# Kernel tuning notes

Hardware: AMD Instinct MI355X
Metric: run time of the kernel (lower is better)

The kernel has to match this reference:

```python
import jax, jax.numpy as jnp
import numpy as np


def setup_inputs() -> dict:
    key = jax.random.key(0)
    ks = jax.random.split(key, 3)
    B, H, W, C = 32, 56, 56, 512
    N = H * W
    x = jax.random.normal(ks[0], (B, N, C), dtype=jnp.float32)
    # learned params (qkv_bias=False)
    w_qkv = jax.random.normal(ks[1], (C, 3 * C), dtype=jnp.float32) * (C ** -0.5)
    w_proj = jax.random.normal(ks[2], (C, C), dtype=jnp.float32) * (C ** -0.5)
    b_proj = jnp.zeros((C,), dtype=jnp.float32)
    return {"x": x, "w_qkv": w_qkv, "w_proj": w_proj, "b_proj": b_proj,
            "H": H, "W": W}


def reference(x, w_qkv, w_proj, b_proj, H, W):
    num_heads, ws = 8, 7
    B, N, C = x.shape
    hd = C // num_heads
    scale = hd ** -0.5
    hg, wg = H // ws, W // ws
    G = hg * wg  # total groups
    S = ws * ws  # tokens per window
    # window partition: [B,N,C] -> [B,G,S,C]
    xw = x.reshape(B, hg, ws, wg, ws, C).transpose(0, 1, 3, 2, 4, 5)
    xw = xw.reshape(B, G, S, C)
    # qkv projection -> [3,B,G,heads,S,hd]
    qkv = (xw @ w_qkv).reshape(B, G, S, 3, num_heads, hd)
    qkv = qkv.transpose(3, 0, 1, 4, 2, 5)
    q, k, v = qkv[0], qkv[1], qkv[2]
    attn = jnp.einsum('bghqd,bghkd->bghqk', q, k) * scale
    attn = jax.nn.softmax(attn, axis=-1)
    out = jnp.einsum('bghqk,bghkd->bghqd', attn, v)
    # merge heads: [B,G,h,S,d] -> [B,G,S,C]
    out = out.transpose(0, 1, 3, 2, 4).reshape(B, G, S, C)
    # window merge: [B,G,S,C] -> [B,N,C]
    out = out.reshape(B, hg, wg, ws, ws, C).transpose(0, 1, 3, 2, 4, 5)
    out = out.reshape(B, N, C)
    return out @ w_proj + b_proj
```

## Files before the change

### kernel.cpp

```cpp
#include <hip/hip_runtime.h>

typedef unsigned short ushort;
typedef unsigned int uint;
typedef __bf16 bf16x8 __attribute__((ext_vector_type(8)));
typedef unsigned short u16x8 __attribute__((ext_vector_type(8)));
typedef float f32x4 __attribute__((ext_vector_type(4)));

__device__ __forceinline__ ushort f2bf(float f) {
  uint u = __builtin_bit_cast(uint, f);
  u += 0x7fffu + ((u >> 16) & 1u);
  return (ushort)(u >> 16);
}

__device__ __forceinline__ f32x4 mfma_bf16(u16x8 a, u16x8 b, f32x4 c) {
  return __builtin_amdgcn_mfma_f32_16x16x32_bf16(
      __builtin_bit_cast(bf16x8, a), __builtin_bit_cast(bf16x8, b), c, 0, 0, 0);
}

__global__ __launch_bounds__(256) void cvt_x(const float* __restrict__ X,
                                             ushort* __restrict__ Xb, int total8) {
  int stride = gridDim.x * 256;
  for (int i = blockIdx.x * 256 + threadIdx.x; i < total8; i += stride) {
    f32x4 a = ((const f32x4*)X)[2 * i];
    f32x4 b = ((const f32x4*)X)[2 * i + 1];
    u16x8 o;
#pragma unroll
    for (int j = 0; j < 4; ++j) { o[j] = f2bf(a[j]); o[j + 4] = f2bf(b[j]); }
    ((u16x8*)Xb)[i] = o;
  }
}

__global__ __launch_bounds__(256) void transpose_cvt(const float* __restrict__ W,
                                                     ushort* __restrict__ WT,
                                                     int K, int N) {
  __shared__ float t[32][33];
  const int tn0 = blockIdx.x * 32, tk0 = blockIdx.y * 32;
  const int tx = threadIdx.x & 31, ty = threadIdx.x >> 5;
#pragma unroll
  for (int i = 0; i < 4; ++i) {
    int k = tk0 + ty + i * 8;
    t[ty + i * 8][tx] = W[(size_t)k * N + tn0 + tx];
  }
  __syncthreads();
#pragma unroll
  for (int i = 0; i < 4; ++i) {
    int n = tn0 + ty + i * 8;
    WT[(size_t)n * K + tk0 + tx] = f2bf(t[tx][ty + i * 8]);
  }
}

__global__ __launch_bounds__(256) void gemm_qkv2(const ushort* __restrict__ A,
                                                 const ushort* __restrict__ BT,
                                                 ushort* __restrict__ C) {
  __shared__ __align__(16) ushort as_[128 * 32];
  __shared__ __align__(16) ushort bs_[128 * 32];
  const int tid = threadIdx.x;
  const int lane = tid & 63;
  const int wid = tid >> 6;
  const int c16 = lane & 15, q4 = lane >> 4;
  const int m0 = blockIdx.x * 128, n0 = blockIdx.y * 128;
  const int wr = (wid >> 1) * 64, wc = (wid & 1) * 64;

  f32x4 acc[4][4];
#pragma unroll
  for (int m = 0; m < 4; ++m)
#pragma unroll
    for (int n = 0; n < 4; ++n) acc[m][n] = f32x4{0.f, 0.f, 0.f, 0.f};

  const ushort* aptr = A + (size_t)(m0 + (tid >> 2)) * 512 + (tid & 3) * 8;
  const ushort* bptr = BT + (size_t)(n0 + (tid >> 2)) * 512 + (tid & 3) * 8;
  auto al0 = (__attribute__((address_space(3))) uint*)(as_ + tid * 8);
  auto al1 = (__attribute__((address_space(3))) uint*)(as_ + 2048 + tid * 8);
  auto bl0 = (__attribute__((address_space(3))) uint*)(bs_ + tid * 8);
  auto bl1 = (__attribute__((address_space(3))) uint*)(bs_ + 2048 + tid * 8);
  const ushort* ard = as_ + (wr + c16) * 32 + q4 * 8;
  const ushort* brd = bs_ + (wc + c16) * 32 + q4 * 8;

  for (int k0 = 0; k0 < 512; k0 += 32) {
    if (k0) __syncthreads();
    __builtin_amdgcn_global_load_lds(
        (__attribute__((address_space(1))) uint*)(aptr + k0), al0, 16, 0, 0);
    __builtin_amdgcn_global_load_lds(
        (__attribute__((address_space(1))) uint*)(aptr + 64 * 512 + k0), al1, 16, 0, 0);
    __builtin_amdgcn_global_load_lds(
        (__attribute__((address_space(1))) uint*)(bptr + k0), bl0, 16, 0, 0);
    __builtin_amdgcn_global_load_lds(
        (__attribute__((address_space(1))) uint*)(bptr + 64 * 512 + k0), bl1, 16, 0, 0);
    __syncthreads();
    u16x8 af[4], bf[4];
#pragma unroll
    for (int m = 0; m < 4; ++m) af[m] = *reinterpret_cast<const u16x8*>(ard + m * 512);
#pragma unroll
    for (int n = 0; n < 4; ++n) bf[n] = *reinterpret_cast<const u16x8*>(brd + n * 512);
#pragma unroll
    for (int m = 0; m < 4; ++m)
#pragma unroll
      for (int n = 0; n < 4; ++n) acc[m][n] = mfma_bf16(af[m], bf[n], acc[m][n]);
  }
  const int row0 = m0 + wr + q4 * 4;
  const int col0 = n0 + wc + c16;
#pragma unroll
  for (int m = 0; m < 4; ++m)
#pragma unroll
    for (int r = 0; r < 4; ++r) {
      ushort* cp = C + (size_t)(row0 + m * 16 + r) * 1536 + col0;
      cp[0]  = f2bf(acc[m][0][r]);
      cp[16] = f2bf(acc[m][1][r]);
      cp[32] = f2bf(acc[m][2][r]);
      cp[48] = f2bf(acc[m][3][r]);
    }
}

__global__ __launch_bounds__(256) void attn_win(const ushort* __restrict__ qkv,
                                                ushort* __restrict__ O) {
  __shared__ __align__(16) ushort p_lds[4][4096];
  __shared__ __align__(16) ushort v_lds[4][4096];
  const int tid = threadIdx.x, lane = tid & 63, w = tid >> 6;
  const int wg = blockIdx.x * 4 + w;
  const int head = wg & 7, g = (wg >> 3) & 63, b = wg >> 9;
  const int gh = g >> 3, gw = g & 7;
  const int c16 = lane & 15, q4 = lane >> 4;
  const size_t brow = (size_t)b * 3136;
  const u16x8 Z = {0, 0, 0, 0, 0, 0, 0, 0};

  int rowq[4]; bool val[4];
#pragma unroll
  for (int i = 0; i < 4; ++i) {
    int s = i * 16 + c16;
    val[i] = (s < 49);
    int ss = val[i] ? s : 0;
    rowq[i] = (gh * 7 + ss / 7) * 56 + gw * 7 + ss % 7;
  }
  const int qc = head * 64 + q4 * 8;

  u16x8 qf[2][4], kf[2][4];
#pragma unroll
  for (int i = 0; i < 4; ++i) {
    const ushort* p = qkv + (brow + rowq[i]) * 1536 + qc;
#pragma unroll
    for (int kk = 0; kk < 2; ++kk) {
      qf[kk][i] = val[i] ? *reinterpret_cast<const u16x8*>(p + kk * 32) : Z;
      kf[kk][i] = val[i] ? *reinterpret_cast<const u16x8*>(p + 512 + kk * 32) : Z;
    }
  }

  {
    int t = lane < 49 ? lane : 0;
    const ushort* vp =
        qkv + (brow + ((gh * 7 + t / 7) * 56 + gw * 7 + t % 7)) * 1536 + 1024 + head * 64;
    u16x8 vr[8];
#pragma unroll
    for (int j = 0; j < 8; ++j)
      vr[j] = (lane < 49) ? *reinterpret_cast<const u16x8*>(vp + j * 8) : Z;
#pragma unroll
    for (int d = 0; d < 64; ++d)
      v_lds[w][(d * 64 + lane) ^ ((d & 7) << 3)] = vr[d >> 3][d & 7];
  }

  f32x4 acc[4][4];
#pragma unroll
  for (int m = 0; m < 4; ++m)
#pragma unroll
    for (int n = 0; n < 4; ++n) acc[m][n] = f32x4{0.f, 0.f, 0.f, 0.f};
#pragma unroll
  for (int kk = 0; kk < 2; ++kk)
#pragma unroll
    for (int m = 0; m < 4; ++m)
#pragma unroll
      for (int n = 0; n < 4; ++n)
        acc[m][n] = mfma_bf16(qf[kk][m], kf[kk][n], acc[m][n]);

#pragma unroll
  for (int m = 0; m < 4; ++m)
#pragma unroll
    for (int r = 0; r < 4; ++r) {
      float s0 = acc[m][0][r] * 0.125f;
      float s1 = acc[m][1][r] * 0.125f;
      float s2 = acc[m][2][r] * 0.125f;
      float s3 = (c16 == 0) ? acc[m][3][r] * 0.125f : -1e30f;
      float mx = fmaxf(fmaxf(s0, s1), fmaxf(s2, s3));
#pragma unroll
      for (int off = 1; off < 16; off <<= 1) mx = fmaxf(mx, __shfl_xor(mx, off));
      s0 = __expf(s0 - mx);
      s1 = __expf(s1 - mx);
      s2 = __expf(s2 - mx);
      s3 = (c16 == 0) ? __expf(s3 - mx) : 0.f;
      float sum = s0 + s1 + s2 + s3;
#pragma unroll
      for (int off = 1; off < 16; off <<= 1) sum += __shfl_xor(sum, off);
      float inv = 1.f / sum;
      int row = m * 16 + q4 * 4 + r;
      int rb = row * 64, sw = (row & 7) << 3;
      p_lds[w][(rb + c16) ^ sw]      = f2bf(s0 * inv);
      p_lds[w][(rb + 16 + c16) ^ sw] = f2bf(s1 * inv);
      p_lds[w][(rb + 32 + c16) ^ sw] = f2bf(s2 * inv);
      p_lds[w][(rb + 48 + c16) ^ sw] = f2bf(s3 * inv);
    }
  __syncthreads();

  f32x4 o[4][4];
#pragma unroll
  for (int m = 0; m < 4; ++m)
#pragma unroll
    for (int n = 0; n < 4; ++n) o[m][n] = f32x4{0.f, 0.f, 0.f, 0.f};
#pragma unroll
  for (int kk = 0; kk < 2; ++kk) {
    u16x8 pa[4], vb[4];
#pragma unroll
    for (int m = 0; m < 4; ++m) {
      int row = m * 16 + c16;
      pa[m] = *reinterpret_cast<const u16x8*>(
          &p_lds[w][(row * 64 + kk * 32 + q4 * 8) ^ ((row & 7) << 3)]);
    }
#pragma unroll
    for (int n = 0; n < 4; ++n) {
      int d = n * 16 + c16;
      vb[n] = *reinterpret_cast<const u16x8*>(
          &v_lds[w][(d * 64 + kk * 32 + q4 * 8) ^ ((d & 7) << 3)]);
    }
#pragma unroll
    for (int m = 0; m < 4; ++m)
#pragma unroll
      for (int n = 0; n < 4; ++n) o[m][n] = mfma_bf16(pa[m], vb[n], o[m][n]);
  }

#pragma unroll
  for (int m = 0; m < 4; ++m)
#pragma unroll
    for (int r = 0; r < 4; ++r) {
      int s = m * 16 + q4 * 4 + r;
      if (s < 49) {
        int n_tok = (gh * 7 + s / 7) * 56 + gw * 7 + s % 7;
        ushort* op = O + (brow + n_tok) * 512 + head * 64 + c16;
        op[0]  = f2bf(o[m][0][r]);
        op[16] = f2bf(o[m][1][r]);
        op[32] = f2bf(o[m][2][r]);
        op[48] = f2bf(o[m][3][r]);
      }
    }
}

__global__ __launch_bounds__(256) void gemm_proj(const ushort* __restrict__ A,
                                                 const ushort* __restrict__ BT,
                                                 const float* __restrict__ bias,
                                                 float* __restrict__ C) {
  __shared__ __align__(16) ushort as_[128 * 32];
  __shared__ __align__(16) ushort bs_[128 * 32];
  const int tid = threadIdx.x;
  const int lane = tid & 63;
  const int wid = tid >> 6;
  const int c16 = lane & 15, q4 = lane >> 4;
  const int m0 = blockIdx.x * 128, n0 = blockIdx.y * 128;
  const int wr = (wid >> 1) * 64, wc = (wid & 1) * 64;

  f32x4 acc[4][4];
#pragma unroll
  for (int m = 0; m < 4; ++m)
#pragma unroll
    for (int n = 0; n < 4; ++n) acc[m][n] = f32x4{0.f, 0.f, 0.f, 0.f};

  const ushort* aptr = A + (size_t)(m0 + (tid >> 2)) * 512 + (tid & 3) * 8;
  const ushort* bptr = BT + (size_t)(n0 + (tid >> 2)) * 512 + (tid & 3) * 8;
  auto al0 = (__attribute__((address_space(3))) uint*)(as_ + tid * 8);
  auto al1 = (__attribute__((address_space(3))) uint*)(as_ + 2048 + tid * 8);
  auto bl0 = (__attribute__((address_space(3))) uint*)(bs_ + tid * 8);
  auto bl1 = (__attribute__((address_space(3))) uint*)(bs_ + 2048 + tid * 8);
  const ushort* ard = as_ + (wr + c16) * 32 + q4 * 8;
  const ushort* brd = bs_ + (wc + c16) * 32 + q4 * 8;

  for (int k0 = 0; k0 < 512; k0 += 32) {
    if (k0) __syncthreads();
    __builtin_amdgcn_global_load_lds(
        (__attribute__((address_space(1))) uint*)(aptr + k0), al0, 16, 0, 0);
    __builtin_amdgcn_global_load_lds(
        (__attribute__((address_space(1))) uint*)(aptr + 64 * 512 + k0), al1, 16, 0, 0);
    __builtin_amdgcn_global_load_lds(
        (__attribute__((address_space(1))) uint*)(bptr + k0), bl0, 16, 0, 0);
    __builtin_amdgcn_global_load_lds(
        (__attribute__((address_space(1))) uint*)(bptr + 64 * 512 + k0), bl1, 16, 0, 0);
    __syncthreads();
    u16x8 af[4], bf[4];
#pragma unroll
    for (int m = 0; m < 4; ++m) af[m] = *reinterpret_cast<const u16x8*>(ard + m * 512);
#pragma unroll
    for (int n = 0; n < 4; ++n) bf[n] = *reinterpret_cast<const u16x8*>(brd + n * 512);
#pragma unroll
    for (int m = 0; m < 4; ++m)
#pragma unroll
      for (int n = 0; n < 4; ++n) acc[m][n] = mfma_bf16(af[m], bf[n], acc[m][n]);
  }
  const int row0 = m0 + wr + q4 * 4;
  const int col0 = n0 + wc + c16;
  const float b0 = bias[col0], b1 = bias[col0 + 16], b2 = bias[col0 + 32], b3 = bias[col0 + 48];
#pragma unroll
  for (int m = 0; m < 4; ++m)
#pragma unroll
    for (int r = 0; r < 4; ++r) {
      float* cp = C + (size_t)(row0 + m * 16 + r) * 512 + col0;
      cp[0]  = acc[m][0][r] + b0;
      cp[16] = acc[m][1][r] + b1;
      cp[32] = acc[m][2][r] + b2;
      cp[48] = acc[m][3][r] + b3;
    }
}

extern "C" void kernel_launch(void* const* d_in, const int* in_sizes, int n_in,
                              void* d_out, int out_size, void* d_ws, size_t ws_size,
                              hipStream_t stream) {
  const float* x      = (const float*)d_in[0];
  const float* w_qkv  = (const float*)d_in[1];
  const float* w_proj = (const float*)d_in[2];
  const float* b_proj = (const float*)d_in[3];
  char* ws = (char*)d_ws;
  ushort* wqkvT  = (ushort*)ws;
  ushort* wprojT = (ushort*)(ws + 1572864);
  ushort* xb     = (ushort*)(ws + 2097152);
  ushort* qkv    = (ushort*)(ws + 104857600);
  float* out = (float*)d_out;

  transpose_cvt<<<dim3(48, 16), 256, 0, stream>>>(w_qkv, wqkvT, 512, 1536);
  transpose_cvt<<<dim3(16, 16), 256, 0, stream>>>(w_proj, wprojT, 512, 512);
  cvt_x<<<2048, 256, 0, stream>>>(x, xb, 100352 * 512 / 8);
  gemm_qkv2<<<dim3(784, 12), 256, 0, stream>>>(xb, wqkvT, qkv);
  attn_win<<<4096, 256, 0, stream>>>(qkv, xb);
  gemm_proj<<<dim3(784, 4), 256, 0, stream>>>(xb, wprojT, b_proj, out);
}
```

Before: 520.7 us.

## Replace GEMMs with 256x256 double-buffered, swizzled, ping-pong pipelined 8-wave kernel

Replaces both 128x128 single-buffered GEMM kernels with one templated 256x256-tile kernel using 8 waves, a BK=64 double-buffered LDS layout with XOR swizzling, and an explicit interleaving of global-to-LDS loads with MFMA phases using waitcnt, barriers and setprio. It also remaps block IDs across XCDs so neighbouring tiles share L2. This aims to hide memory latency and improve arithmetic intensity in the QKV and output projections. The risks are the fragile hand-tuned vmcnt counts and the larger LDS footprint, which limits occupancy.

```diff
diff --git a/kernel.cpp b/kernel.cpp
--- a/kernel.cpp
+++ b/kernel.cpp
@@ -49,66 +49,167 @@
   }
 }
 
-__global__ __launch_bounds__(256) void gemm_qkv2(const ushort* __restrict__ A,
+
+#define GLL(g, l)                                                              \
+  __builtin_amdgcn_global_load_lds(                                            \
+      (const __attribute__((address_space(1))) uint*)(g),                      \
+      (__attribute__((address_space(3))) uint*)(l), 16, 0, 0)
+#define BAR() __builtin_amdgcn_s_barrier()
+#define SCB() __builtin_amdgcn_sched_barrier(0)
+#define WAITV(n) asm volatile("s_waitcnt vmcnt(" #n ")" ::: "memory")
+
+template <int OUT>
+__global__ __launch_bounds__(512, 2) void gemm8p(const ushort* __restrict__ A,
                                                  const ushort* __restrict__ BT,
-                                                 ushort* __restrict__ C) {
-  __shared__ __align__(16) ushort as_[128 * 32];
-  __shared__ __align__(16) ushort bs_[128 * 32];
-  const int tid = threadIdx.x;
-  const int lane = tid & 63;
-  const int wid = tid >> 6;
+                                                 void* __restrict__ Cout,
+                                                 const float* __restrict__ bias,
+                                                 const int ldc, const int NT,
+                                                 const int CPX) {
+  __shared__ __align__(16) ushort as_[2][16384];
+  __shared__ __align__(16) ushort bs_[2][16384];
+  const int bid = blockIdx.x;
+  const int wg = (bid & 7) * CPX + (bid >> 3);
+  const int mt = wg / NT, nt = wg - mt * NT;
+  const int m0 = mt << 8, n0 = nt << 8;
+  const int tid = threadIdx.x, lane = tid & 63, wid = tid >> 6;
+  const int wm = wid >> 2, wn = wid & 3;
   const int c16 = lane & 15, q4 = lane >> 4;
-  const int m0 = blockIdx.x * 128, n0 = blockIdx.y * 128;
-  const int wr = (wid >> 1) * 64, wc = (wid & 1) * 64;
-
-  f32x4 acc[4][4];
-#pragma unroll
-  for (int m = 0; m < 4; ++m)
+  const int sw = c16 & 7;
+  const int lrow = lane >> 3, lcg = (lane & 7) ^ lrow;
+  const ushort* Ag = A + (size_t)(m0 + wid * 16 + lrow) * 512 + lcg * 8;
+  const ushort* Bg = BT + (size_t)(n0 + wid * 16 + lrow) * 512 + lcg * 8;
+  const int aro = (wm * 64 + c16) * 64;
+  const int bro = (wn * 32 + c16) * 64;
+  const int ag0 = (q4 ^ sw) * 8;
+  const int ag1 = ((4 + q4) ^ sw) * 8;
+
+  f32x4 acc[8][4];
+#pragma unroll
+  for (int m = 0; m < 8; ++m)
 #pragma unroll
     for (int n = 0; n < 4; ++n) acc[m][n] = f32x4{0.f, 0.f, 0.f, 0.f};
-
-  const ushort* aptr = A + (size_t)(m0 + (tid >> 2)) * 512 + (tid & 3) * 8;
-  const ushort* bptr = BT + (size_t)(n0 + (tid >> 2)) * 512 + (tid & 3) * 8;
-  auto al0 = (__attribute__((address_space(3))) uint*)(as_ + tid * 8);
-  auto al1 = (__attribute__((address_space(3))) uint*)(as_ + 2048 + tid * 8);
-  auto bl0 = (__attribute__((address_space(3))) uint*)(bs_ + tid * 8);
-  auto bl1 = (__attribute__((address_space(3))) uint*)(bs_ + 2048 + tid * 8);
-  const ushort* ard = as_ + (wr + c16) * 32 + q4 * 8;
-  const ushort* brd = bs_ + (wc + c16) * 32 + q4 * 8;
-
-  for (int k0 = 0; k0 < 512; k0 += 32) {
-    if (k0) __syncthreads();
-    __builtin_amdgcn_global_load_lds(
-        (__attribute__((address_space(1))) uint*)(aptr + k0), al0, 16, 0, 0);
-    __builtin_amdgcn_global_load_lds(
-        (__attribute__((address_space(1))) uint*)(aptr + 64 * 512 + k0), al1, 16, 0, 0);
-    __builtin_amdgcn_global_load_lds(
-        (__attribute__((address_space(1))) uint*)(bptr + k0), bl0, 16, 0, 0);
-    __builtin_amdgcn_global_load_lds(
-        (__attribute__((address_space(1))) uint*)(bptr + 64 * 512 + k0), bl1, 16, 0, 0);
-    __syncthreads();
-    u16x8 af[4], bf[4];
-#pragma unroll
-    for (int m = 0; m < 4; ++m) af[m] = *reinterpret_cast<const u16x8*>(ard + m * 512);
-#pragma unroll
-    for (int n = 0; n < 4; ++n) bf[n] = *reinterpret_cast<const u16x8*>(brd + n * 512);
-#pragma unroll
-    for (int m = 0; m < 4; ++m)
-#pragma unroll
-      for (int n = 0; n < 4; ++n) acc[m][n] = mfma_bf16(af[m], bf[n], acc[m][n]);
-  }
-  const int row0 = m0 + wr + q4 * 4;
-  const int col0 = n0 + wc + c16;
-#pragma unroll
-  for (int m = 0; m < 4; ++m)
-#pragma unroll
-    for (int r = 0; r < 4; ++r) {
-      ushort* cp = C + (size_t)(row0 + m * 16 + r) * 1536 + col0;
-      cp[0]  = f2bf(acc[m][0][r]);
-      cp[16] = f2bf(acc[m][1][r]);
-      cp[32] = f2bf(acc[m][2][r]);
-      cp[48] = f2bf(acc[m][3][r]);
-    }
+  u16x8 af[4][2], bf0[2][2], bf1[2][2];
+
+#define STAGE_A(half, ktg)                                                     \
+  do {                                                                         \
+    const ushort* g_ = Ag + (size_t)(half) * (128 * 512) + (ktg) * 64;         \
+    ushort* l_ = &as_[(ktg) & 1][(half) * 8192 + wid * 1024 + lane * 8];       \
+    GLL(g_, l_);                                                               \
+    GLL(g_ + 8 * 512, l_ + 512);                                               \
+  } while (0)
+#define STAGE_B(half, ktg)                                                     \
+  do {                                                                         \
+    const ushort* g_ = Bg + (size_t)(half) * (128 * 512) + (ktg) * 64;         \
+    ushort* l_ = &bs_[(ktg) & 1][(half) * 8192 + wid * 1024 + lane * 8];       \
+    GLL(g_, l_);                                                               \
+    GLL(g_ + 8 * 512, l_ + 512);                                               \
+  } while (0)
+#define LDA(kt, mh)                                                            \
+  do {                                                                         \
+    const ushort* p_ = &as_[kt][(mh)*8192 + aro];                              \
+    _Pragma("unroll") for (int f_ = 0; f_ < 4; ++f_) {                         \
+      af[f_][0] = *(const u16x8*)(p_ + f_ * 1024 + ag0);                       \
+      af[f_][1] = *(const u16x8*)(p_ + f_ * 1024 + ag1);                       \
+    }                                                                          \
+  } while (0)
+#define LDB(kt, nh, BF)                                                        \
+  do {                                                                         \
+    const ushort* p_ = &bs_[kt][(nh)*8192 + bro];                              \
+    _Pragma("unroll") for (int g_ = 0; g_ < 2; ++g_) {                         \
+      BF[g_][0] = *(const u16x8*)(p_ + g_ * 1024 + ag0);                       \
+      BF[g_][1] = *(const u16x8*)(p_ + g_ * 1024 + ag1);                       \
+    }                                                                          \
+  } while (0)
+#define MM(mh, nh, BF)                                                         \
+  do {                                                                         \
+    __builtin_amdgcn_s_setprio(1);                                             \
+    _Pragma("unroll") for (int f_ = 0; f_ < 4; ++f_)                           \
+        _Pragma("unroll") for (int g_ = 0; g_ < 2; ++g_) {                     \
+      f32x4& a_ = acc[(mh)*4 + f_][(nh)*2 + g_];                               \
+      a_ = mfma_bf16(af[f_][0], BF[g_][0], a_);                                \
+      a_ = mfma_bf16(af[f_][1], BF[g_][1], a_);                                \
+    }                                                                          \
+    __builtin_amdgcn_s_setprio(0);                                             \
+  } while (0)
+
+  STAGE_A(0, 0); STAGE_B(1, 0); STAGE_B(0, 0);
+  STAGE_A(1, 0); STAGE_A(0, 1); STAGE_B(1, 1);
+  WAITV(6); BAR(); SCB();
+
+  for (int i = 0; i < 3; ++i) {
+    const int k1g = 2 * i + 1, k2g = 2 * i + 2, k3g = 2 * i + 3;
+    LDA(0, 0); LDB(0, 0, bf0); STAGE_A(1, k1g);
+    BAR(); MM(0, 0, bf0); WAITV(10); BAR(); SCB();
+    LDB(0, 1, bf1); STAGE_B(0, k1g);
+    BAR(); MM(0, 1, bf1); WAITV(8); BAR(); SCB();
+    LDA(0, 1); STAGE_A(0, k2g);
+    BAR(); MM(1, 1, bf1); BAR(); SCB();
+    STAGE_B(1, k2g);
+    BAR(); MM(1, 0, bf0); WAITV(4); BAR(); SCB();
+    LDA(1, 0); LDB(1, 0, bf0); STAGE_B(0, k2g);
+    BAR(); MM(0, 0, bf0); WAITV(10); BAR(); SCB();
+    LDB(1, 1, bf1); STAGE_A(1, k2g);
+    BAR(); MM(0, 1, bf1); WAITV(10); BAR(); SCB();
+    LDA(1, 1); STAGE_A(0, k3g);
+    BAR(); MM(1, 1, bf1); BAR(); SCB();
+    STAGE_B(1, k3g);
+    BAR(); MM(1, 0, bf0); WAITV(6); BAR(); SCB();
+  }
+  {
+    LDA(0, 0); LDB(0, 0, bf0); STAGE_A(1, 7);
+    BAR(); MM(0, 0, bf0); WAITV(10); BAR(); SCB();
+    LDB(0, 1, bf1); STAGE_B(0, 7);
+    BAR(); MM(0, 1, bf1); WAITV(8); BAR(); SCB();
+    LDA(0, 1);
+    BAR(); MM(1, 1, bf1); BAR(); SCB();
+    BAR(); MM(1, 0, bf0); WAITV(0); BAR(); SCB();
+    LDA(1, 0); LDB(1, 0, bf0);
+    BAR(); MM(0, 0, bf0); BAR(); SCB();
+    LDB(1, 1, bf1);
+    BAR(); MM(0, 1, bf1); BAR(); SCB();
+    LDA(1, 1);
+    BAR(); MM(1, 1, bf1); BAR(); SCB();
+    BAR(); MM(1, 0, bf0);
+  }
+
+  const int crow = m0 + wm * 64 + q4 * 4;
+  const int ccol = n0 + wn * 32 + c16;
+  if constexpr (OUT == 0) {
+    ushort* C = (ushort*)Cout;
+#pragma unroll
+    for (int mf = 0; mf < 8; ++mf) {
+      const int ro = (mf >> 2) * 128 + (mf & 3) * 16;
+#pragma unroll
+      for (int r = 0; r < 4; ++r) {
+        ushort* cp = C + (size_t)(crow + ro + r) * ldc + ccol;
+        cp[0]   = f2bf(acc[mf][0][r]);
+        cp[16]  = f2bf(acc[mf][1][r]);
+        cp[128] = f2bf(acc[mf][2][r]);
+        cp[144] = f2bf(acc[mf][3][r]);
+      }
+    }
+  } else {
+    float* C = (float*)Cout;
+    const float b0 = bias[ccol], b1 = bias[ccol + 16];
+    const float b2 = bias[ccol + 128], b3 = bias[ccol + 144];
+#pragma unroll
+    for (int mf = 0; mf < 8; ++mf) {
+      const int ro = (mf >> 2) * 128 + (mf & 3) * 16;
+#pragma unroll
+      for (int r = 0; r < 4; ++r) {
+        float* cp = C + (size_t)(crow + ro + r) * ldc + ccol;
+        cp[0]   = acc[mf][0][r] + b0;
+        cp[16]  = acc[mf][1][r] + b1;
+        cp[128] = acc[mf][2][r] + b2;
+        cp[144] = acc[mf][3][r] + b3;
+      }
+    }
+  }
+#undef STAGE_A
+#undef STAGE_B
+#undef LDA
+#undef LDB
+#undef MM
 }
 
 __global__ __launch_bounds__(256) void attn_win(const ushort* __restrict__ qkv,
@@ -237,70 +338,6 @@
         op[32] = f2bf(o[m][2][r]);
         op[48] = f2bf(o[m][3][r]);
       }
-    }
-}
-
-__global__ __launch_bounds__(256) void gemm_proj(const ushort* __restrict__ A,
-                                                 const ushort* __restrict__ BT,
-                                                 const float* __restrict__ bias,
-                                                 float* __restrict__ C) {
-  __shared__ __align__(16) ushort as_[128 * 32];
-  __shared__ __align__(16) ushort bs_[128 * 32];
-  const int tid = threadIdx.x;
-  const int lane = tid & 63;
-  const int wid = tid >> 6;
-  const int c16 = lane & 15, q4 = lane >> 4;
-  const int m0 = blockIdx.x * 128, n0 = blockIdx.y * 128;
-  const int wr = (wid >> 1) * 64, wc = (wid & 1) * 64;
-
-  f32x4 acc[4][4];
-#pragma unroll
-  for (int m = 0; m < 4; ++m)
-#pragma unroll
-    for (int n = 0; n < 4; ++n) acc[m][n] = f32x4{0.f, 0.f, 0.f, 0.f};
-
-  const ushort* aptr = A + (size_t)(m0 + (tid >> 2)) * 512 + (tid & 3) * 8;
-  const ushort* bptr = BT + (size_t)(n0 + (tid >> 2)) * 512 + (tid & 3) * 8;
-  auto al0 = (__attribute__((address_space(3))) uint*)(as_ + tid * 8);
-  auto al1 = (__attribute__((address_space(3))) uint*)(as_ + 2048 + tid * 8);
-  auto bl0 = (__attribute__((address_space(3))) uint*)(bs_ + tid * 8);
-  auto bl1 = (__attribute__((address_space(3))) uint*)(bs_ + 2048 + tid * 8);
-  const ushort* ard = as_ + (wr + c16) * 32 + q4 * 8;
-  const ushort* brd = bs_ + (wc + c16) * 32 + q4 * 8;
-
-  for (int k0 = 0; k0 < 512; k0 += 32) {
-    if (k0) __syncthreads();
-    __builtin_amdgcn_global_load_lds(
-        (__attribute__((address_space(1))) uint*)(aptr + k0), al0, 16, 0, 0);
-    __builtin_amdgcn_global_load_lds(
-        (__attribute__((address_space(1))) uint*)(aptr + 64 * 512 + k0), al1, 16, 0, 0);
-    __builtin_amdgcn_global_load_lds(
-        (__attribute__((address_space(1))) uint*)(bptr + k0), bl0, 16, 0, 0);
-    __builtin_amdgcn_global_load_lds(
-        (__attribute__((address_space(1))) uint*)(bptr + 64 * 512 + k0), bl1, 16, 0, 0);
-    __syncthreads();
-    u16x8 af[4], bf[4];
-#pragma unroll
-    for (int m = 0; m < 4; ++m) af[m] = *reinterpret_cast<const u16x8*>(ard + m * 512);
-#pragma unroll
-    for (int n = 0; n < 4; ++n) bf[n] = *reinterpret_cast<const u16x8*>(brd + n * 512);
-#pragma unroll
-    for (int m = 0; m < 4; ++m)
-#pragma unroll
-      for (int n = 0; n < 4; ++n) acc[m][n] = mfma_bf16(af[m], bf[n], acc[m][n]);
-  }
-  const int row0 = m0 + wr + q4 * 4;
-  const int col0 = n0 + wc + c16;
-  const float b0 = bias[col0], b1 = bias[col0 + 16], b2 = bias[col0 + 32], b3 = bias[col0 + 48];
-#pragma unroll
-  for (int m = 0; m < 4; ++m)
-#pragma unroll
-    for (int r = 0; r < 4; ++r) {
-      float* cp = C + (size_t)(row0 + m * 16 + r) * 512 + col0;
-      cp[0]  = acc[m][0][r] + b0;
-      cp[16] = acc[m][1][r] + b1;
-      cp[32] = acc[m][2][r] + b2;
-      cp[48] = acc[m][3][r] + b3;
     }
 }
 
@@ -321,7 +358,7 @@
   transpose_cvt<<<dim3(48, 16), 256, 0, stream>>>(w_qkv, wqkvT, 512, 1536);
   transpose_cvt<<<dim3(16, 16), 256, 0, stream>>>(w_proj, wprojT, 512, 512);
   cvt_x<<<2048, 256, 0, stream>>>(x, xb, 100352 * 512 / 8);
-  gemm_qkv2<<<dim3(784, 12), 256, 0, stream>>>(xb, wqkvT, qkv);
+  gemm8p<0><<<2352, 512, 0, stream>>>(xb, wqkvT, (void*)qkv, nullptr, 1536, 6, 294);
   attn_win<<<4096, 256, 0, stream>>>(qkv, xb);
-  gemm_proj<<<dim3(784, 4), 256, 0, stream>>>(xb, wprojT, b_proj, out);
-}
+  gemm8p<1><<<784, 512, 0, stream>>>(xb, wprojT, (void*)out, b_proj, 512, 2, 98);
+}
```

Measured after the change: 488.5 us. 1.07x faster.
